# Kernel tuning notes

Hardware: AMD Instinct MI355X
Metric: run time of the kernel (lower is better)

The kernel has to match this reference:

```python
import jax, jax.numpy as jnp
import numpy as np

N = 500000        # total atoms (n1 nodes)
G = 20000         # graphs (g nodes)
D_IN = 128        # in_features
D_H = 256         # hidden width (config_local / mid_features)
D_OUT = 1         # final output per graph (config_global last int)


def setup_inputs() -> dict:
    key = jax.random.key(0)
    ks = jax.random.split(key, 10)
    h = jax.random.normal(ks[0], (N, D_IN), dtype=jnp.float32)
    graph_ids = jnp.sort(jax.random.randint(ks[1], (N,), 0, G))
    s = 0.05
    return {
        "h": h,
        "graph_ids": graph_ids,
        "num_graphs": G,
        # d_local: Linear(128->256) relu, Linear(256->256) relu
        "W1": jax.random.normal(ks[2], (D_IN, D_H), dtype=jnp.float32) * s,
        "b1": jnp.zeros((D_H,), dtype=jnp.float32),
        "W2": jax.random.normal(ks[3], (D_H, D_H), dtype=jnp.float32) * s,
        "b2": jnp.zeros((D_H,), dtype=jnp.float32),
        # d_global: Linear(256->256) relu, Linear(256->1)
        "Wg1": jax.random.normal(ks[4], (D_H, D_H), dtype=jnp.float32) * s,
        "bg1": jnp.zeros((D_H,), dtype=jnp.float32),
        "Wg2": jax.random.normal(ks[5], (D_H, D_OUT), dtype=jnp.float32) * s,
        "bg2": jnp.zeros((D_OUT,), dtype=jnp.float32),
    }


def reference(h, graph_ids, num_graphs, W1, b1, W2, b2, Wg1, bg1, Wg2, bg2):
    # node-level MLP (d_local): h_global per n1 node
    x = jax.nn.relu(h @ W1 + b1)            # [N, D_H]
    x = jax.nn.relu(x @ W2 + b2)            # [N, D_H]
    # copy_src + sum over n1_in_g edges == per-graph segment sum
    pooled = jax.ops.segment_sum(x, graph_ids, num_segments=num_graphs)  # [G, D_H]
    # graph-level MLP (d_global)
    y = jax.nn.relu(pooled @ Wg1 + bg1)     # [G, D_H]
    return y @ Wg2 + bg2                    # [G, 1]
```

## Files before the change

### kernel.cpp

```cpp
#include <hip/hip_runtime.h>
#include <stdint.h>

#define D_IN 128
#define D_H  256
#define BM   64
#define BMG  64

typedef float f32x4 __attribute__((ext_vector_type(4)));
typedef short s16x8 __attribute__((ext_vector_type(8)));
typedef unsigned int u32x2 __attribute__((ext_vector_type(2)));
typedef unsigned int u32x4 __attribute__((ext_vector_type(4)));

__device__ __forceinline__ unsigned short f2bf(float x) {
  union { float f; uint32_t u; } v; v.f = x;
  uint32_t r = v.u + 0x7fffu + ((v.u >> 16) & 1u);
  return (unsigned short)(r >> 16);
}
__device__ __forceinline__ float bf2f(unsigned short u) {
  union { uint32_t u; float f; } v; v.u = (uint32_t)u << 16;
  return v.f;
}
__device__ __forceinline__ uint32_t pkbf(float lo, float hi) {
#if __has_builtin(__builtin_amdgcn_cvt_pk_bf16_f32)
  auto r = __builtin_amdgcn_cvt_pk_bf16_f32(lo, hi);
  uint32_t u; __builtin_memcpy(&u, &r, 4); return u;
#else
  return (uint32_t)f2bf(lo) | ((uint32_t)f2bf(hi) << 16);
#endif
}

__global__ void prep_kernel(const float* __restrict__ W1, const float* __restrict__ W2,
                            const float* __restrict__ Wg1,
                            float* __restrict__ pooled, unsigned short* __restrict__ W1t,
                            unsigned short* __restrict__ W2t, unsigned short* __restrict__ Wg1t,
                            int pooled_n) {
  int stride = gridDim.x * blockDim.x;
  int tid = blockIdx.x * blockDim.x + threadIdx.x;
  float4 z4 = make_float4(0.f, 0.f, 0.f, 0.f);
  for (int i = tid; i < (pooled_n >> 2); i += stride) ((float4*)pooled)[i] = z4;
  for (int i = tid; i < D_H * D_IN; i += stride) {
    int n = i >> 7, k = i & (D_IN - 1);
    W1t[i] = f2bf(W1[k * D_H + n]);
  }
  for (int i = tid; i < D_H * D_H; i += stride) {
    int n = i >> 8, k = i & (D_H - 1);
    W2t[i]  = f2bf(W2[k * D_H + n]);
    Wg1t[i] = f2bf(Wg1[k * D_H + n]);
  }
}

__global__ __launch_bounds__(256, 4)
void node_kernel(const float* __restrict__ h, const int* __restrict__ gids,
                 const float* __restrict__ b1, const float* __restrict__ b2,
                 const unsigned short* __restrict__ W1t, const unsigned short* __restrict__ W2t,
                 float* __restrict__ pooled, int nnodes) {
  __shared__ unsigned short buf[BM * D_H];
  __shared__ int sgid[BM];
  const int tid  = threadIdx.x;
  const int lane = tid & 63;
  const int wave = tid >> 6;
  const int lr   = lane & 15;
  const int q    = lane >> 4;
  const int row0 = blockIdx.x * BM;
  unsigned short* hA = buf + 8192;

  const unsigned short* w1base = W1t + (wave * 64 + lr) * D_IN + q * 8;
  const unsigned short* w2base = W2t + (wave * 64 + lr) * D_H + q * 8;

  s16x8 a[2][4];
  #pragma unroll
  for (int mt = 0; mt < 4; ++mt) a[0][mt] = *(const s16x8*)(w1base + mt * 16 * D_IN + 0 * 32);
  #pragma unroll
  for (int mt = 0; mt < 4; ++mt) a[1][mt] = *(const s16x8*)(w1base + mt * 16 * D_IN + 1 * 32);

  if (tid < BM) {
    int gr = row0 + tid;
    sgid[tid] = (gr < nnodes) ? gids[gr] : -1;
  }

  #pragma unroll
  for (int i = 0; i < 4; ++i) {
    int gi = tid + i * 256, r = gi >> 4, gc = gi & 15, gr = row0 + r;
    f32x4 v0 = (f32x4){0.f, 0.f, 0.f, 0.f}, v1 = v0;
    if (gr < nnodes) {
      const f32x4* p = (const f32x4*)(h + (size_t)gr * D_IN + gc * 8);
      v0 = __builtin_nontemporal_load(p);
      v1 = __builtin_nontemporal_load(p + 1);
    }
    u32x4 u;
    u[0] = pkbf(v0[0], v0[1]); u[1] = pkbf(v0[2], v0[3]);
    u[2] = pkbf(v1[0], v1[1]); u[3] = pkbf(v1[2], v1[3]);
    *(u32x4*)&hA[r * D_IN + ((gc ^ (r & 7)) << 3)] = u;
  }
  __syncthreads();

  f32x4 acc[4][4];
  #pragma unroll
  for (int mt = 0; mt < 4; ++mt)
    #pragma unroll
    for (int nt = 0; nt < 4; ++nt)
      acc[mt][nt] = (f32x4){0.f, 0.f, 0.f, 0.f};

  #pragma unroll
  for (int ks = 0; ks < 4; ++ks) {
    const int kq = ks * 32 + q * 8;
    s16x8 b[4];
    #pragma unroll
    for (int nt = 0; nt < 4; ++nt)
      b[nt] = *(const s16x8*)&hA[(nt * 16 + lr) * D_IN + (((kq >> 3) ^ (lr & 7)) << 3)];
    #pragma unroll
    for (int mt = 0; mt < 4; ++mt)
      #pragma unroll
      for (int nt = 0; nt < 4; ++nt)
        acc[mt][nt] = __builtin_amdgcn_mfma_f32_16x16x32_bf16(a[ks & 1][mt], b[nt], acc[mt][nt], 0, 0, 0);
    if (ks < 2) {
      #pragma unroll
      for (int mt = 0; mt < 4; ++mt)
        a[ks & 1][mt] = *(const s16x8*)(w1base + mt * 16 * D_IN + (ks + 2) * 32);
    } else {
      #pragma unroll
      for (int mt = 0; mt < 4; ++mt)
        a[ks & 1][mt] = *(const s16x8*)(w2base + mt * 16 * D_H + (ks - 2) * 32);
    }
  }

  __syncthreads();

  #pragma unroll
  for (int mt = 0; mt < 4; ++mt) {
    int f = wave * 64 + mt * 16 + q * 4;
    float4 bias = *(const float4*)&b1[f];
    #pragma unroll
    for (int nt = 0; nt < 4; ++nt) {
      int nd = nt * 16 + lr;
      u32x2 w;
      w[0] = pkbf(fmaxf(acc[mt][nt][0] + bias.x, 0.f), fmaxf(acc[mt][nt][1] + bias.y, 0.f));
      w[1] = pkbf(fmaxf(acc[mt][nt][2] + bias.z, 0.f), fmaxf(acc[mt][nt][3] + bias.w, 0.f));
      *(u32x2*)&buf[nd * D_H + (((f >> 3) ^ (nd & 7)) << 3) + (f & 7)] = w;
    }
  }
  __syncthreads();

  #pragma unroll
  for (int mt = 0; mt < 4; ++mt)
    #pragma unroll
    for (int nt = 0; nt < 4; ++nt)
      acc[mt][nt] = (f32x4){0.f, 0.f, 0.f, 0.f};

  #pragma unroll
  for (int ks = 0; ks < 8; ++ks) {
    const int kq = ks * 32 + q * 8;
    s16x8 b[4];
    #pragma unroll
    for (int nt = 0; nt < 4; ++nt)
      b[nt] = *(const s16x8*)&buf[(nt * 16 + lr) * D_H + (((kq >> 3) ^ (lr & 7)) << 3)];
    #pragma unroll
    for (int mt = 0; mt < 4; ++mt)
      #pragma unroll
      for (int nt = 0; nt < 4; ++nt)
        acc[mt][nt] = __builtin_amdgcn_mfma_f32_16x16x32_bf16(a[ks & 1][mt], b[nt], acc[mt][nt], 0, 0, 0);
    if (ks < 6) {
      #pragma unroll
      for (int mt = 0; mt < 4; ++mt)
        a[ks & 1][mt] = *(const s16x8*)(w2base + mt * 16 * D_H + (ks + 2) * 32);
    }
  }
  __syncthreads();

  #pragma unroll
  for (int mt = 0; mt < 4; ++mt) {
    int f = wave * 64 + mt * 16 + q * 4;
    float4 bias = *(const float4*)&b2[f];
    #pragma unroll
    for (int nt = 0; nt < 4; ++nt) {
      int nd = nt * 16 + lr;
      u32x2 w;
      w[0] = pkbf(fmaxf(acc[mt][nt][0] + bias.x, 0.f), fmaxf(acc[mt][nt][1] + bias.y, 0.f));
      w[1] = pkbf(fmaxf(acc[mt][nt][2] + bias.z, 0.f), fmaxf(acc[mt][nt][3] + bias.w, 0.f));
      *(u32x2*)&buf[nd * D_H + (((f >> 3) ^ (nd & 7)) << 3) + (f & 7)] = w;
    }
  }

  {
    const int f0  = wave * 64 + (lane & 15) * 4;
    const int rg  = lane >> 4;
    const int swz = f0 >> 3;
    const int sub = f0 & 7;
    float ra0 = 0.f, ra1 = 0.f, ra2 = 0.f, ra3 = 0.f;
    for (int rr = 0; rr < 16; ++rr) {
      int r = rg * 16 + rr;
      int g = sgid[r];
      if (g >= 0) {
        u32x2 wv = *(const u32x2*)&buf[r * D_H + ((swz ^ (r & 7)) << 3) + sub];
        ra0 += bf2f((unsigned short)(wv[0] & 0xffffu));
        ra1 += bf2f((unsigned short)(wv[0] >> 16));
        ra2 += bf2f((unsigned short)(wv[1] & 0xffffu));
        ra3 += bf2f((unsigned short)(wv[1] >> 16));
        if (rr == 15 || sgid[r + 1] != g) {
          float* dst = &pooled[g * D_H + f0];
          atomicAdd(dst + 0, ra0);
          atomicAdd(dst + 1, ra1);
          atomicAdd(dst + 2, ra2);
          atomicAdd(dst + 3, ra3);
          ra0 = ra1 = ra2 = ra3 = 0.f;
        }
      }
    }
  }
}

__global__ __launch_bounds__(256, 4)
void graph_kernel(const float* __restrict__ pooled, const float* __restrict__ bg1,
                  const unsigned short* __restrict__ Wg1t, const float* __restrict__ Wg2,
                  const float* __restrict__ bg2, float* __restrict__ out, int ngraphs) {
  __shared__ unsigned short pA[BMG * D_H];
  const int tid  = threadIdx.x;
  const int lane = tid & 63;
  const int wave = tid >> 6;
  const int lr   = lane & 15;
  const int q    = lane >> 4;
  const int g0   = blockIdx.x * BMG;

  #pragma unroll
  for (int i = 0; i < 8; ++i) {
    int gi = tid + i * 256, r = gi >> 5, gc = gi & 31;
    int gr = g0 + r;
    f32x4 v0 = (f32x4){0.f, 0.f, 0.f, 0.f}, v1 = v0;
    if (gr < ngraphs) {
      const f32x4* p = (const f32x4*)(pooled + (size_t)gr * D_H + gc * 8);
      v0 = p[0]; v1 = p[1];
    }
    u32x4 u;
    u[0] = pkbf(v0[0], v0[1]); u[1] = pkbf(v0[2], v0[3]);
    u[2] = pkbf(v1[0], v1[1]); u[3] = pkbf(v1[2], v1[3]);
    *(u32x4*)&pA[r * D_H + (((gc & 7) ^ (r & 7)) << 3) + ((gc & 24) << 3)] = u;
  }
  __syncthreads();

  f32x4 acc[4][4];
  #pragma unroll
  for (int mt = 0; mt < 4; ++mt)
    #pragma unroll
    for (int nt = 0; nt < 4; ++nt)
      acc[mt][nt] = (f32x4){0.f, 0.f, 0.f, 0.f};

  #pragma unroll
  for (int ks = 0; ks < 8; ++ks) {
    const int kq = ks * 32 + q * 8;
    s16x8 a[4], b[4];
    #pragma unroll
    for (int mt = 0; mt < 4; ++mt)
      a[mt] = *(const s16x8*)&Wg1t[(wave * 64 + mt * 16 + lr) * D_H + kq];
    #pragma unroll
    for (int nt = 0; nt < 4; ++nt) {
      int row = nt * 16 + lr, gw = kq >> 3;
      b[nt] = *(const s16x8*)&pA[row * D_H + (((gw & 7) ^ (row & 7)) << 3) + ((gw & 24) << 3)];
    }
    #pragma unroll
    for (int mt = 0; mt < 4; ++mt)
      #pragma unroll
      for (int nt = 0; nt < 4; ++nt)
        acc[mt][nt] = __builtin_amdgcn_mfma_f32_16x16x32_bf16(a[mt], b[nt], acc[mt][nt], 0, 0, 0);
  }
  __syncthreads();

  #pragma unroll
  for (int mt = 0; mt < 4; ++mt) {
    int f = wave * 64 + mt * 16 + q * 4;
    float4 bias = *(const float4*)&bg1[f];
    #pragma unroll
    for (int nt = 0; nt < 4; ++nt) {
      int nd = nt * 16 + lr;
      u32x2 w;
      w[0] = pkbf(fmaxf(acc[mt][nt][0] + bias.x, 0.f), fmaxf(acc[mt][nt][1] + bias.y, 0.f));
      w[1] = pkbf(fmaxf(acc[mt][nt][2] + bias.z, 0.f), fmaxf(acc[mt][nt][3] + bias.w, 0.f));
      int gw = f >> 3;
      *(u32x2*)&pA[nd * D_H + (((gw & 7) ^ (nd & 7)) << 3) + ((gw & 24) << 3) + (f & 7)] = w;
    }
  }
  __syncthreads();

  int gloc = tid >> 2;
  int part = tid & 3;
  float p = 0.f;
  #pragma unroll 8
  for (int i = 0; i < 32; ++i) {
    int f2 = part + 4 * i;
    int hw = 2 * f2;
    int gw = hw >> 3;
    uint32_t wv = *(const uint32_t*)&pA[gloc * D_H + (((gw & 7) ^ (gloc & 7)) << 3) +
                                        ((gw & 24) << 3) + (hw & 7)];
    float2 wg = ((const float2*)Wg2)[f2];
    p += bf2f((unsigned short)(wv & 0xffffu)) * wg.x +
         bf2f((unsigned short)(wv >> 16)) * wg.y;
  }
  p += __shfl_xor(p, 1);
  p += __shfl_xor(p, 2);
  if (part == 0 && (g0 + gloc) < ngraphs)
    out[g0 + gloc] = p + bg2[0];
}

extern "C" void kernel_launch(void* const* d_in, const int* in_sizes, int n_in,
                              void* d_out, int out_size, void* d_ws, size_t ws_size,
                              hipStream_t stream) {
  const float* h   = (const float*)d_in[0];
  const int*   gid = (const int*)d_in[1];
  const float* W1  = (const float*)d_in[3];
  const float* b1  = (const float*)d_in[4];
  const float* W2  = (const float*)d_in[5];
  const float* b2  = (const float*)d_in[6];
  const float* Wg1 = (const float*)d_in[7];
  const float* bg1 = (const float*)d_in[8];
  const float* Wg2 = (const float*)d_in[9];
  const float* bg2 = (const float*)d_in[10];
  float* out = (float*)d_out;

  const int N = in_sizes[1];
  const int G = out_size;

  char* ws = (char*)d_ws;
  float* pooled = (float*)ws;
  size_t off = (size_t)G * D_H * sizeof(float);
  unsigned short* W1t  = (unsigned short*)(ws + off); off += (size_t)D_H * D_IN * 2;
  unsigned short* W2t  = (unsigned short*)(ws + off); off += (size_t)D_H * D_H * 2;
  unsigned short* Wg1t = (unsigned short*)(ws + off);

  prep_kernel<<<512, 256, 0, stream>>>(W1, W2, Wg1, pooled, W1t, W2t, Wg1t, G * D_H);
  node_kernel<<<(N + BM - 1) / BM, 256, 0, stream>>>(h, gid, b1, b2, W1t, W2t, pooled, N);
  graph_kernel<<<(G + BMG - 1) / BMG, 256, 0, stream>>>(pooled, bg1, Wg1t, Wg2, bg2, out, G);
}
```

Baseline: 633.8 us.

## Make node kernel persistent with register prefetch of next tile

Converts the node MLP kernel into a persistent kernel with a fixed grid of 768 blocks. Each block walks a contiguous range of 64-row tiles. The next tile's h rows, graph ids and W1 fragments are loaded into registers during the current tile's pooling phase, so global-load latency overlaps compute. Weight fragments are now held four k-steps deep instead of double-buffered, raising register pressure, so launch bounds drop to 3 blocks per CU. This risks lower occupancy and spills in exchange for fewer block launches and hidden load latency.

After: 907.9 us. +43.2%, slower.

```diff
diff --git a/kernel.cpp b/kernel.cpp
--- a/kernel.cpp
+++ b/kernel.cpp
@@ -49,11 +49,11 @@
   }
 }
 
-__global__ __launch_bounds__(256, 4)
+__global__ __launch_bounds__(256, 3)
 void node_kernel(const float* __restrict__ h, const int* __restrict__ gids,
                  const float* __restrict__ b1, const float* __restrict__ b2,
                  const unsigned short* __restrict__ W1t, const unsigned short* __restrict__ W2t,
-                 float* __restrict__ pooled, int nnodes) {
+                 float* __restrict__ pooled, int nnodes, int ntiles) {
   __shared__ unsigned short buf[BM * D_H];
   __shared__ int sgid[BM];
   const int tid  = threadIdx.x;
@@ -61,148 +61,200 @@
   const int wave = tid >> 6;
   const int lr   = lane & 15;
   const int q    = lane >> 4;
-  const int row0 = blockIdx.x * BM;
   unsigned short* hA = buf + 8192;
+
+  const int t0 = (int)(((long long)blockIdx.x * ntiles) / gridDim.x);
+  const int t1 = (int)(((long long)(blockIdx.x + 1) * ntiles) / gridDim.x);
+  if (t0 >= t1) return;
 
   const unsigned short* w1base = W1t + (wave * 64 + lr) * D_IN + q * 8;
   const unsigned short* w2base = W2t + (wave * 64 + lr) * D_H + q * 8;
 
-  s16x8 a[2][4];
-  #pragma unroll
-  for (int mt = 0; mt < 4; ++mt) a[0][mt] = *(const s16x8*)(w1base + mt * 16 * D_IN + 0 * 32);
-  #pragma unroll
-  for (int mt = 0; mt < 4; ++mt) a[1][mt] = *(const s16x8*)(w1base + mt * 16 * D_IN + 1 * 32);
-
-  if (tid < BM) {
-    int gr = row0 + tid;
-    sgid[tid] = (gr < nnodes) ? gids[gr] : -1;
-  }
-
-  #pragma unroll
-  for (int i = 0; i < 4; ++i) {
-    int gi = tid + i * 256, r = gi >> 4, gc = gi & 15, gr = row0 + r;
-    f32x4 v0 = (f32x4){0.f, 0.f, 0.f, 0.f}, v1 = v0;
-    if (gr < nnodes) {
-      const f32x4* p = (const f32x4*)(h + (size_t)gr * D_IN + gc * 8);
-      v0 = __builtin_nontemporal_load(p);
-      v1 = __builtin_nontemporal_load(p + 1);
-    }
-    u32x4 u;
-    u[0] = pkbf(v0[0], v0[1]); u[1] = pkbf(v0[2], v0[3]);
-    u[2] = pkbf(v1[0], v1[1]); u[3] = pkbf(v1[2], v1[3]);
-    *(u32x4*)&hA[r * D_IN + ((gc ^ (r & 7)) << 3)] = u;
-  }
-  __syncthreads();
-
-  f32x4 acc[4][4];
-  #pragma unroll
-  for (int mt = 0; mt < 4; ++mt)
-    #pragma unroll
-    for (int nt = 0; nt < 4; ++nt)
-      acc[mt][nt] = (f32x4){0.f, 0.f, 0.f, 0.f};
-
-  #pragma unroll
-  for (int ks = 0; ks < 4; ++ks) {
-    const int kq = ks * 32 + q * 8;
-    s16x8 b[4];
-    #pragma unroll
-    for (int nt = 0; nt < 4; ++nt)
-      b[nt] = *(const s16x8*)&hA[(nt * 16 + lr) * D_IN + (((kq >> 3) ^ (lr & 7)) << 3)];
+  s16x8 a[4][4];
+  f32x4 hr[4][2];
+  int gcur = -1;
+
+  {
+    const int row0 = t0 * BM;
+    #pragma unroll
+    for (int ks = 0; ks < 4; ++ks)
+      #pragma unroll
+      for (int mt = 0; mt < 4; ++mt)
+        a[ks][mt] = *(const s16x8*)(w1base + mt * 16 * D_IN + ks * 32);
+    #pragma unroll
+    for (int i = 0; i < 4; ++i) {
+      int gi = tid + i * 256, r = gi >> 4, gc = gi & 15, gr = row0 + r;
+      hr[i][0] = (f32x4){0.f, 0.f, 0.f, 0.f}; hr[i][1] = hr[i][0];
+      if (gr < nnodes) {
+        const f32x4* p = (const f32x4*)(h + (size_t)gr * D_IN + gc * 8);
+        hr[i][0] = __builtin_nontemporal_load(p);
+        hr[i][1] = __builtin_nontemporal_load(p + 1);
+      }
+    }
+    if (tid < BM) {
+      int gr = row0 + tid;
+      gcur = (gr < nnodes) ? gids[gr] : -1;
+    }
+  }
+
+  for (int t = t0; t < t1; ++t) {
+    if (t > t0) __syncthreads();
+
+    if (tid < BM) sgid[tid] = gcur;
+
+    #pragma unroll
+    for (int i = 0; i < 4; ++i) {
+      int gi = tid + i * 256, r = gi >> 4, gc = gi & 15;
+      u32x4 u;
+      u[0] = pkbf(hr[i][0][0], hr[i][0][1]); u[1] = pkbf(hr[i][0][2], hr[i][0][3]);
+      u[2] = pkbf(hr[i][1][0], hr[i][1][1]); u[3] = pkbf(hr[i][1][2], hr[i][1][3]);
+      *(u32x4*)&hA[r * D_IN + ((gc ^ (r & 7)) << 3)] = u;
+    }
+    __syncthreads();
+
+    f32x4 acc[4][4];
     #pragma unroll
     for (int mt = 0; mt < 4; ++mt)
       #pragma unroll
       for (int nt = 0; nt < 4; ++nt)
-        acc[mt][nt] = __builtin_amdgcn_mfma_f32_16x16x32_bf16(a[ks & 1][mt], b[nt], acc[mt][nt], 0, 0, 0);
-    if (ks < 2) {
-      #pragma unroll
-      for (int mt = 0; mt < 4; ++mt)
-        a[ks & 1][mt] = *(const s16x8*)(w1base + mt * 16 * D_IN + (ks + 2) * 32);
-    } else {
-      #pragma unroll
-      for (int mt = 0; mt < 4; ++mt)
-        a[ks & 1][mt] = *(const s16x8*)(w2base + mt * 16 * D_H + (ks - 2) * 32);
-    }
-  }
-
-  __syncthreads();
-
-  #pragma unroll
-  for (int mt = 0; mt < 4; ++mt) {
-    int f = wave * 64 + mt * 16 + q * 4;
-    float4 bias = *(const float4*)&b1[f];
-    #pragma unroll
-    for (int nt = 0; nt < 4; ++nt) {
-      int nd = nt * 16 + lr;
-      u32x2 w;
-      w[0] = pkbf(fmaxf(acc[mt][nt][0] + bias.x, 0.f), fmaxf(acc[mt][nt][1] + bias.y, 0.f));
-      w[1] = pkbf(fmaxf(acc[mt][nt][2] + bias.z, 0.f), fmaxf(acc[mt][nt][3] + bias.w, 0.f));
-      *(u32x2*)&buf[nd * D_H + (((f >> 3) ^ (nd & 7)) << 3) + (f & 7)] = w;
-    }
-  }
-  __syncthreads();
-
-  #pragma unroll
-  for (int mt = 0; mt < 4; ++mt)
-    #pragma unroll
-    for (int nt = 0; nt < 4; ++nt)
-      acc[mt][nt] = (f32x4){0.f, 0.f, 0.f, 0.f};
-
-  #pragma unroll
-  for (int ks = 0; ks < 8; ++ks) {
-    const int kq = ks * 32 + q * 8;
-    s16x8 b[4];
-    #pragma unroll
-    for (int nt = 0; nt < 4; ++nt)
-      b[nt] = *(const s16x8*)&buf[(nt * 16 + lr) * D_H + (((kq >> 3) ^ (lr & 7)) << 3)];
+        acc[mt][nt] = (f32x4){0.f, 0.f, 0.f, 0.f};
+
+    #pragma unroll
+    for (int ks = 0; ks < 4; ++ks) {
+      const int kq = ks * 32 + q * 8;
+      s16x8 b[4];
+      #pragma unroll
+      for (int nt = 0; nt < 4; ++nt)
+        b[nt] = *(const s16x8*)&hA[(nt * 16 + lr) * D_IN + (((kq >> 3) ^ (lr & 7)) << 3)];
+      #pragma unroll
+      for (int mt = 0; mt < 4; ++mt)
+        #pragma unroll
+        for (int nt = 0; nt < 4; ++nt)
+          acc[mt][nt] = __builtin_amdgcn_mfma_f32_16x16x32_bf16(a[ks][mt], b[nt], acc[mt][nt], 0, 0, 0);
+    }
+
+    #pragma unroll
+    for (int ks = 0; ks < 4; ++ks)
+      #pragma unroll
+      for (int mt = 0; mt < 4; ++mt)
+        a[ks][mt] = *(const s16x8*)(w2base + mt * 16 * D_H + ks * 32);
+
+    __syncthreads();
+
+    #pragma unroll
+    for (int mt = 0; mt < 4; ++mt) {
+      int f = wave * 64 + mt * 16 + q * 4;
+      float4 bias = *(const float4*)&b1[f];
+      #pragma unroll
+      for (int nt = 0; nt < 4; ++nt) {
+        int nd = nt * 16 + lr;
+        u32x2 w;
+        w[0] = pkbf(fmaxf(acc[mt][nt][0] + bias.x, 0.f), fmaxf(acc[mt][nt][1] + bias.y, 0.f));
+        w[1] = pkbf(fmaxf(acc[mt][nt][2] + bias.z, 0.f), fmaxf(acc[mt][nt][3] + bias.w, 0.f));
+        *(u32x2*)&buf[nd * D_H + (((f >> 3) ^ (nd & 7)) << 3) + (f & 7)] = w;
+      }
+    }
+    __syncthreads();
+
     #pragma unroll
     for (int mt = 0; mt < 4; ++mt)
       #pragma unroll
       for (int nt = 0; nt < 4; ++nt)
-        acc[mt][nt] = __builtin_amdgcn_mfma_f32_16x16x32_bf16(a[ks & 1][mt], b[nt], acc[mt][nt], 0, 0, 0);
-    if (ks < 6) {
-      #pragma unroll
-      for (int mt = 0; mt < 4; ++mt)
-        a[ks & 1][mt] = *(const s16x8*)(w2base + mt * 16 * D_H + (ks + 2) * 32);
-    }
-  }
-  __syncthreads();
-
-  #pragma unroll
-  for (int mt = 0; mt < 4; ++mt) {
-    int f = wave * 64 + mt * 16 + q * 4;
-    float4 bias = *(const float4*)&b2[f];
-    #pragma unroll
-    for (int nt = 0; nt < 4; ++nt) {
-      int nd = nt * 16 + lr;
-      u32x2 w;
-      w[0] = pkbf(fmaxf(acc[mt][nt][0] + bias.x, 0.f), fmaxf(acc[mt][nt][1] + bias.y, 0.f));
-      w[1] = pkbf(fmaxf(acc[mt][nt][2] + bias.z, 0.f), fmaxf(acc[mt][nt][3] + bias.w, 0.f));
-      *(u32x2*)&buf[nd * D_H + (((f >> 3) ^ (nd & 7)) << 3) + (f & 7)] = w;
-    }
-  }
-
-  {
-    const int f0  = wave * 64 + (lane & 15) * 4;
-    const int rg  = lane >> 4;
-    const int swz = f0 >> 3;
-    const int sub = f0 & 7;
-    float ra0 = 0.f, ra1 = 0.f, ra2 = 0.f, ra3 = 0.f;
-    for (int rr = 0; rr < 16; ++rr) {
-      int r = rg * 16 + rr;
-      int g = sgid[r];
-      if (g >= 0) {
-        u32x2 wv = *(const u32x2*)&buf[r * D_H + ((swz ^ (r & 7)) << 3) + sub];
-        ra0 += bf2f((unsigned short)(wv[0] & 0xffffu));
-        ra1 += bf2f((unsigned short)(wv[0] >> 16));
-        ra2 += bf2f((unsigned short)(wv[1] & 0xffffu));
-        ra3 += bf2f((unsigned short)(wv[1] >> 16));
-        if (rr == 15 || sgid[r + 1] != g) {
-          float* dst = &pooled[g * D_H + f0];
-          atomicAdd(dst + 0, ra0);
-          atomicAdd(dst + 1, ra1);
-          atomicAdd(dst + 2, ra2);
-          atomicAdd(dst + 3, ra3);
-          ra0 = ra1 = ra2 = ra3 = 0.f;
+        acc[mt][nt] = (f32x4){0.f, 0.f, 0.f, 0.f};
+
+    #pragma unroll
+    for (int ks = 0; ks < 4; ++ks) {
+      const int kq = ks * 32 + q * 8;
+      s16x8 b[4];
+      #pragma unroll
+      for (int nt = 0; nt < 4; ++nt)
+        b[nt] = *(const s16x8*)&buf[(nt * 16 + lr) * D_H + (((kq >> 3) ^ (lr & 7)) << 3)];
+      #pragma unroll
+      for (int mt = 0; mt < 4; ++mt)
+        #pragma unroll
+        for (int nt = 0; nt < 4; ++nt)
+          acc[mt][nt] = __builtin_amdgcn_mfma_f32_16x16x32_bf16(a[ks][mt], b[nt], acc[mt][nt], 0, 0, 0);
+    }
+    #pragma unroll
+    for (int ks = 0; ks < 4; ++ks)
+      #pragma unroll
+      for (int mt = 0; mt < 4; ++mt)
+        a[ks][mt] = *(const s16x8*)(w2base + mt * 16 * D_H + 128 + ks * 32);
+    #pragma unroll
+    for (int ks = 0; ks < 4; ++ks) {
+      const int kq = 128 + ks * 32 + q * 8;
+      s16x8 b[4];
+      #pragma unroll
+      for (int nt = 0; nt < 4; ++nt)
+        b[nt] = *(const s16x8*)&buf[(nt * 16 + lr) * D_H + (((kq >> 3) ^ (lr & 7)) << 3)];
+      #pragma unroll
+      for (int mt = 0; mt < 4; ++mt)
+        #pragma unroll
+        for (int nt = 0; nt < 4; ++nt)
+          acc[mt][nt] = __builtin_amdgcn_mfma_f32_16x16x32_bf16(a[ks][mt], b[nt], acc[mt][nt], 0, 0, 0);
+    }
+    __syncthreads();
+
+    #pragma unroll
+    for (int mt = 0; mt < 4; ++mt) {
+      int f = wave * 64 + mt * 16 + q * 4;
+      float4 bias = *(const float4*)&b2[f];
+      #pragma unroll
+      for (int nt = 0; nt < 4; ++nt) {
+        int nd = nt * 16 + lr;
+        u32x2 w;
+        w[0] = pkbf(fmaxf(acc[mt][nt][0] + bias.x, 0.f), fmaxf(acc[mt][nt][1] + bias.y, 0.f));
+        w[1] = pkbf(fmaxf(acc[mt][nt][2] + bias.z, 0.f), fmaxf(acc[mt][nt][3] + bias.w, 0.f));
+        *(u32x2*)&buf[nd * D_H + (((f >> 3) ^ (nd & 7)) << 3) + (f & 7)] = w;
+      }
+    }
+
+    if (t + 1 < t1) {
+      const int row0n = (t + 1) * BM;
+      #pragma unroll
+      for (int ks = 0; ks < 4; ++ks)
+        #pragma unroll
+        for (int mt = 0; mt < 4; ++mt)
+          a[ks][mt] = *(const s16x8*)(w1base + mt * 16 * D_IN + ks * 32);
+      #pragma unroll
+      for (int i = 0; i < 4; ++i) {
+        int gi = tid + i * 256, r = gi >> 4, gc = gi & 15, gr = row0n + r;
+        hr[i][0] = (f32x4){0.f, 0.f, 0.f, 0.f}; hr[i][1] = hr[i][0];
+        if (gr < nnodes) {
+          const f32x4* p = (const f32x4*)(h + (size_t)gr * D_IN + gc * 8);
+          hr[i][0] = __builtin_nontemporal_load(p);
+          hr[i][1] = __builtin_nontemporal_load(p + 1);
+        }
+      }
+      if (tid < BM) {
+        int gr = row0n + tid;
+        gcur = (gr < nnodes) ? gids[gr] : -1;
+      }
+    }
+
+    {
+      const int f0  = wave * 64 + (lane & 15) * 4;
+      const int rg  = lane >> 4;
+      const int swz = f0 >> 3;
+      const int sub = f0 & 7;
+      float ra0 = 0.f, ra1 = 0.f, ra2 = 0.f, ra3 = 0.f;
+      for (int rr = 0; rr < 16; ++rr) {
+        int r = rg * 16 + rr;
+        int g = sgid[r];
+        if (g >= 0) {
+          u32x2 wv = *(const u32x2*)&buf[r * D_H + ((swz ^ (r & 7)) << 3) + sub];
+          ra0 += bf2f((unsigned short)(wv[0] & 0xffffu));
+          ra1 += bf2f((unsigned short)(wv[0] >> 16));
+          ra2 += bf2f((unsigned short)(wv[1] & 0xffffu));
+          ra3 += bf2f((unsigned short)(wv[1] >> 16));
+          if (rr == 15 || sgid[r + 1] != g) {
+            float* dst = &pooled[g * D_H + f0];
+            atomicAdd(dst + 0, ra0);
+            atomicAdd(dst + 1, ra1);
+            atomicAdd(dst + 2, ra2);
+            atomicAdd(dst + 3, ra3);
+            ra0 = ra1 = ra2 = ra3 = 0.f;
+          }
         }
       }
     }
@@ -325,7 +377,11 @@
   unsigned short* W2t  = (unsigned short*)(ws + off); off += (size_t)D_H * D_H * 2;
   unsigned short* Wg1t = (unsigned short*)(ws + off);
 
+  const int ntiles = (N + BM - 1) / BM;
+  int grid = 3 * 256;
+  if (grid > ntiles) grid = ntiles;
+
   prep_kernel<<<512, 256, 0, stream>>>(W1, W2, Wg1, pooled, W1t, W2t, Wg1t, G * D_H);
-  node_kernel<<<(N + BM - 1) / BM, 256, 0, stream>>>(h, gid, b1, b2, W1t, W2t, pooled, N);
+  node_kernel<<<grid, 256, 0, stream>>>(h, gid, b1, b2, W1t, W2t, pooled, N, ntiles);
   graph_kernel<<<(G + BMG - 1) / BMG, 256, 0, stream>>>(pooled, bg1, Wg1t, Wg2, bg2, out, G);
 }
```
